# Kernel tuning notes

Measured on AMD Instinct MI355X. Metric: run time of the kernel, lower is better.

## Reference

```python
import jax, jax.numpy as jnp
import numpy as np

IN_DIM = 512
OUT_DIM = 128


def setup_inputs() -> dict:
    key = jax.random.key(0)
    ks = jax.random.split(key, 10)
    B, H, W = 8, 64, 64
    s_in = 1.0 / np.sqrt(IN_DIM)
    s_out = 1.0 / np.sqrt(OUT_DIM)
    return {
        "x": jax.random.normal(ks[0], (B, IN_DIM, H, W), dtype=jnp.float32),
        "W_in": jax.random.normal(ks[1], (OUT_DIM, IN_DIM), dtype=jnp.float32) * s_in,
        "b_in": jax.random.normal(ks[2], (OUT_DIM,), dtype=jnp.float32) * s_in,
        "W_q": jax.random.normal(ks[3], (OUT_DIM, OUT_DIM), dtype=jnp.float32) * s_out,
        "b_q": jax.random.normal(ks[4], (OUT_DIM,), dtype=jnp.float32) * s_out,
        "W_k": jax.random.normal(ks[5], (OUT_DIM, OUT_DIM), dtype=jnp.float32) * s_out,
        "b_k": jax.random.normal(ks[6], (OUT_DIM,), dtype=jnp.float32) * s_out,
        "W_v": jax.random.normal(ks[7], (OUT_DIM, OUT_DIM), dtype=jnp.float32) * s_out,
        "b_v": jax.random.normal(ks[8], (OUT_DIM,), dtype=jnp.float32) * s_out,
        "gamma": jax.random.normal(ks[9], (1,), dtype=jnp.float32) * 0.1,
    }


def reference(x, W_in, b_in, W_q, b_q, W_k, b_k, W_v, b_v, gamma):
    # 1x1 input projection: (B, C_in, H, W) -> (B, C, H, W)
    x = jnp.einsum('bihw,oi->bohw', x, W_in) + b_in[None, :, None, None]
    B, C, H, W = x.shape
    N = H * W
    xf = x.reshape(B, C, N)
    # 1x1 convs on flattened spatial dim are per-token matmuls
    q = jnp.einsum('bcn,oc->bon', xf, W_q) + b_q[None, :, None]  # (B, C, N)
    k = jnp.einsum('bcn,oc->bon', xf, W_k) + b_k[None, :, None]
    v = jnp.einsum('bcn,oc->bon', xf, W_v) + b_v[None, :, None]
    # energy[b, n, m] = sum_c q[b, c, n] * k[b, c, m]   (no 1/sqrt(d) scaling)
    energy = jnp.einsum('bcn,bcm->bnm', q, k)
    attention = jax.nn.softmax(energy, axis=-1)  # (B, N, N)
    # out[b, c, n] = sum_m v[b, c, m] * attention[b, n, m]  (V @ A^T)
    out = jnp.einsum('bcm,bnm->bcn', v, attention).reshape(B, C, H, W)
    return gamma * out + x
```

## Files before the change

kernel.cpp:

```cpp
#include <hip/hip_runtime.h>


typedef __attribute__((ext_vector_type(4))) float f32x4;
typedef __attribute__((ext_vector_type(8))) short bf16x8;
typedef __attribute__((ext_vector_type(4))) unsigned short u16x4;

#define MFMA16(a, b, c) __builtin_amdgcn_mfma_f32_16x16x32_bf16((a), (b), (c), 0, 0, 0)
#define LOG2E 1.44269504088896340736f
#define SOFTMAX_SHIFT 40.0f

#if __has_builtin(__builtin_amdgcn_exp2f)
#define EXP2F(x) __builtin_amdgcn_exp2f(x)
#else
#define EXP2F(x) exp2f(x)
#endif

__device__ __forceinline__ unsigned short f2bf(float f) {
  union { float f; unsigned int u; } v; v.f = f;
  unsigned int r = v.u + 0x7FFFu + ((v.u >> 16) & 1u);
  return (unsigned short)(r >> 16);
}

__device__ __forceinline__ void gload_lds16(const void* g, void* l) {
  __builtin_amdgcn_global_load_lds(
      (const __attribute__((address_space(1))) unsigned int*)(unsigned long long)g,
      (__attribute__((address_space(3))) unsigned int*)(unsigned int)(unsigned long long)l,
      16, 0, 0);
}

__global__ void cvt_w_kernel(const float* __restrict__ Win, const float* __restrict__ Wq,
                             const float* __restrict__ Wk, const float* __restrict__ Wv,
                             unsigned short* __restrict__ o) {
  int t = blockIdx.x * 256 + threadIdx.x;
  if (t < 65536)       o[t] = f2bf(Win[t]);
  else if (t < 81920)  o[t] = f2bf(Wq[t - 65536]);
  else if (t < 98304)  o[t] = f2bf(Wk[t - 81920]);
  else if (t < 114688) o[t] = f2bf(Wv[t - 98304]);
}

__global__ __launch_bounds__(256) void proj_in_kernel(
    const float* __restrict__ x, const unsigned short* __restrict__ Wb,
    const float* __restrict__ b_in, float* __restrict__ xf, unsigned short* __restrict__ xh) {
  __shared__ alignas(16) unsigned short xt[16 * 512];
  const int tid = threadIdx.x;
  const int w = tid >> 6, L = tid & 63, l15 = L & 15, qd = L >> 4;
  const int n0 = blockIdx.x * 64;
  const int b = blockIdx.y;
  const float* xb = x + (size_t)b * 512 * 4096;

  f32x4 acc[2][4];
#pragma unroll
  for (int ma = 0; ma < 2; ++ma)
#pragma unroll
    for (int nb = 0; nb < 4; ++nb) acc[ma][nb] = (f32x4){0.f, 0.f, 0.f, 0.f};

  for (int c4 = 0; c4 < 4; ++c4) {
    const int i0 = c4 * 128;
    __syncthreads();
    {
      const int nl = (tid & 15) * 4;
#pragma unroll
      for (int it = 0; it < 8; ++it) {
        const int il = (tid >> 4) + it * 16;
        f32x4 xv = *(const f32x4*)(xb + (size_t)(i0 + il) * 4096 + n0 + nl);
        const int kk = il >> 5, qr = (il >> 3) & 3, j = il & 7;
#pragma unroll
        for (int jj = 0; jj < 4; ++jj) {
          const int n_local = nl + jj;
          xt[(((n_local >> 4) << 2) + kk) * 512 + (qr * 16 + (n_local & 15)) * 8 + j] =
              f2bf(xv[jj]);
        }
      }
    }
    __syncthreads();
#pragma unroll
    for (int kk = 0; kk < 4; ++kk) {
      bf16x8 a[2];
#pragma unroll
      for (int ma = 0; ma < 2; ++ma)
        a[ma] = *(const bf16x8*)(Wb + (size_t)(w * 32 + ma * 16 + l15) * 512 + i0 + kk * 32 + qd * 8);
#pragma unroll
      for (int nb = 0; nb < 4; ++nb) {
        bf16x8 bf = *(const bf16x8*)&xt[(nb * 4 + kk) * 512 + L * 8];
#pragma unroll
        for (int ma = 0; ma < 2; ++ma) acc[ma][nb] = MFMA16(a[ma], bf, acc[ma][nb]);
      }
    }
  }
  float* xfb = xf + (size_t)b * 128 * 4096;
  unsigned short* xhb = xh + (size_t)b * 4096 * 128;
#pragma unroll
  for (int ma = 0; ma < 2; ++ma) {
    const int c0 = w * 32 + ma * 16 + qd * 4;
    const float bi0 = b_in[c0], bi1 = b_in[c0 + 1], bi2 = b_in[c0 + 2], bi3 = b_in[c0 + 3];
#pragma unroll
    for (int nb = 0; nb < 4; ++nb) {
      const int n = n0 + nb * 16 + l15;
      const float v0 = acc[ma][nb][0] + bi0, v1 = acc[ma][nb][1] + bi1;
      const float v2 = acc[ma][nb][2] + bi2, v3 = acc[ma][nb][3] + bi3;
      xfb[(size_t)(c0 + 0) * 4096 + n] = v0;
      xfb[(size_t)(c0 + 1) * 4096 + n] = v1;
      xfb[(size_t)(c0 + 2) * 4096 + n] = v2;
      xfb[(size_t)(c0 + 3) * 4096 + n] = v3;
      u16x4 h = {f2bf(v0), f2bf(v1), f2bf(v2), f2bf(v3)};
      *(u16x4*)&xhb[(size_t)n * 128 + c0] = h;
    }
  }
}

__global__ __launch_bounds__(256) void proj_qkv_kernel(
    const unsigned short* __restrict__ xh, const unsigned short* __restrict__ Wq,
    const float* __restrict__ bq, const unsigned short* __restrict__ Wk,
    const float* __restrict__ bk, const unsigned short* __restrict__ Wv,
    const float* __restrict__ bv, unsigned short* __restrict__ qt,
    unsigned short* __restrict__ kt, unsigned short* __restrict__ vv) {
  __shared__ alignas(16) unsigned short xt[32 * 512];
  const int tid = threadIdx.x;
  const int w = tid >> 6, L = tid & 63, l15 = L & 15, qd = L >> 4;
  const int n0 = blockIdx.x * 128;
  const int b = blockIdx.y;
  const unsigned short* xhb = xh + (size_t)b * 4096 * 128;

#pragma unroll
  for (int j = 0; j < 8; ++j) {
    const int blk = w * 8 + j;
    const int nb = blk >> 2, kk = blk & 3;
    const unsigned short* g = xhb + (size_t)(n0 + nb * 16 + l15) * 128 + kk * 32 + qd * 8;
    gload_lds16(g, &xt[blk * 512]);
  }
  __syncthreads();

  for (int which = 0; which < 2; ++which) {
    const unsigned short* W = which ? Wk : Wq;
    const float* bias = which ? bk : bq;
    unsigned short* dst = (which ? kt : qt) + (size_t)b * 4096 * 128;
    f32x4 acc[2][8];
#pragma unroll
    for (int ma = 0; ma < 2; ++ma)
#pragma unroll
      for (int nb = 0; nb < 8; ++nb) acc[ma][nb] = (f32x4){0.f, 0.f, 0.f, 0.f};
#pragma unroll
    for (int kk = 0; kk < 4; ++kk) {
      bf16x8 a[2];
#pragma unroll
      for (int ma = 0; ma < 2; ++ma)
        a[ma] = *(const bf16x8*)(W + (size_t)(w * 32 + ma * 16 + l15) * 128 + kk * 32 + qd * 8);
#pragma unroll
      for (int nb = 0; nb < 8; ++nb) {
        bf16x8 bf = *(const bf16x8*)&xt[(nb * 4 + kk) * 512 + L * 8];
#pragma unroll
        for (int ma = 0; ma < 2; ++ma) acc[ma][nb] = MFMA16(a[ma], bf, acc[ma][nb]);
      }
    }
#pragma unroll
    for (int ma = 0; ma < 2; ++ma) {
      const int c0 = w * 32 + ma * 16 + qd * 4;
      const float b0 = bias[c0], b1 = bias[c0 + 1], b2 = bias[c0 + 2], b3 = bias[c0 + 3];
#pragma unroll
      for (int nb = 0; nb < 8; ++nb) {
        const int n = n0 + nb * 16 + l15;
        u16x4 h = {f2bf(acc[ma][nb][0] + b0), f2bf(acc[ma][nb][1] + b1),
                   f2bf(acc[ma][nb][2] + b2), f2bf(acc[ma][nb][3] + b3)};
        *(u16x4*)&dst[(size_t)n * 128 + c0] = h;
      }
    }
  }
  {
    f32x4 acc[2][8];
#pragma unroll
    for (int ma = 0; ma < 2; ++ma)
#pragma unroll
      for (int cb = 0; cb < 8; ++cb) acc[ma][cb] = (f32x4){0.f, 0.f, 0.f, 0.f};
#pragma unroll
    for (int kk = 0; kk < 4; ++kk) {
      bf16x8 a[2];
#pragma unroll
      for (int ma = 0; ma < 2; ++ma)
        a[ma] = *(const bf16x8*)&xt[(((w * 2 + ma) << 2) + kk) * 512 + L * 8];
#pragma unroll
      for (int cb = 0; cb < 8; ++cb) {
        bf16x8 bf = *(const bf16x8*)(Wv + (size_t)(cb * 16 + l15) * 128 + kk * 32 + qd * 8);
#pragma unroll
        for (int ma = 0; ma < 2; ++ma) acc[ma][cb] = MFMA16(a[ma], bf, acc[ma][cb]);
      }
    }
    unsigned short* db = vv + (size_t)b * 128 * 4096;
#pragma unroll
    for (int ma = 0; ma < 2; ++ma) {
      const int nbase = n0 + w * 32 + ma * 16 + qd * 4;
#pragma unroll
      for (int cb = 0; cb < 8; ++cb) {
        const int c = cb * 16 + l15;
        const float bvv = bv[c];
        u16x4 h = {f2bf(acc[ma][cb][0] + bvv), f2bf(acc[ma][cb][1] + bvv),
                   f2bf(acc[ma][cb][2] + bvv), f2bf(acc[ma][cb][3] + bvv)};
        *(u16x4*)&db[(size_t)c * 4096 + nbase] = h;
      }
    }
  }
}

__global__ __launch_bounds__(256, 2) void attn_kernel(
    const unsigned short* __restrict__ qt, const unsigned short* __restrict__ kt,
    const unsigned short* __restrict__ vv, float* __restrict__ pa,
    float* __restrict__ lp, int nsplit) {
  __shared__ alignas(16) unsigned short kbuf[16 * 512];
  __shared__ alignas(16) unsigned short vbuf[16 * 512];
  __shared__ alignas(16) unsigned short pbuf[4][32][72];

  const int tid = threadIdx.x;
  const int w = tid >> 6, L = tid & 63, l15 = L & 15, qd = L >> 4;
  const int bidx = blockIdx.x;
  const int b = bidx & 7;
  const int r2 = bidx >> 3;
  const int qtile = r2 & 31, split = r2 >> 5;
  const int n00 = qtile * 128;
  const int mlen = 4096 / nsplit;
  const int mbeg = split * mlen;

  const unsigned short* qtb = qt + (size_t)b * 4096 * 128;
  const unsigned short* ktb = kt + (size_t)b * 4096 * 128;
  const unsigned short* vvb = vv + (size_t)b * 128 * 4096;

  bf16x8 qf[2][4];
#pragma unroll
  for (int nh = 0; nh < 2; ++nh) {
    const unsigned short* qrow = qtb + (size_t)(n00 + w * 32 + nh * 16 + l15) * 128 + qd * 8;
#pragma unroll
    for (int kk = 0; kk < 4; ++kk) qf[nh][kk] = *(const bf16x8*)(qrow + kk * 32);
  }

  f32x4 acc[2][8];
#pragma unroll
  for (int nh = 0; nh < 2; ++nh)
#pragma unroll
    for (int cb = 0; cb < 8; ++cb) acc[nh][cb] = (f32x4){0.f, 0.f, 0.f, 0.f};
  float lsum[2] = {0.f, 0.f};
  const float sb = SOFTMAX_SHIFT * LOG2E;

  for (int m0 = mbeg; m0 < mbeg + mlen; m0 += 64) {
    __syncthreads();
#pragma unroll
    for (int j = 0; j < 4; ++j) {
      const int blk = w * 4 + j;
      const int mb = blk >> 2, kk = blk & 3;
      gload_lds16(ktb + (size_t)(m0 + mb * 16 + l15) * 128 + kk * 32 + qd * 8,
                  &kbuf[blk * 512]);
      const int cb2 = blk >> 1, kkm = blk & 1;
      gload_lds16(vvb + (size_t)(cb2 * 16 + l15) * 4096 + m0 + kkm * 32 + qd * 8,
                  &vbuf[blk * 512]);
    }
    __syncthreads();

    f32x4 s[2][4];
#pragma unroll
    for (int mb = 0; mb < 4; ++mb) {
      s[0][mb] = (f32x4){0.f, 0.f, 0.f, 0.f};
      s[1][mb] = (f32x4){0.f, 0.f, 0.f, 0.f};
#pragma unroll
      for (int kk = 0; kk < 4; ++kk) {
        bf16x8 kf = *(const bf16x8*)&kbuf[(mb * 4 + kk) * 512 + L * 8];
        s[0][mb] = MFMA16(kf, qf[0][kk], s[0][mb]);
        s[1][mb] = MFMA16(kf, qf[1][kk], s[1][mb]);
      }
    }
#pragma unroll
    for (int nh = 0; nh < 2; ++nh) {
#pragma unroll
      for (int mb = 0; mb < 4; ++mb) {
        float p0 = EXP2F(__builtin_fmaf(s[nh][mb][0], LOG2E, -sb));
        float p1 = EXP2F(__builtin_fmaf(s[nh][mb][1], LOG2E, -sb));
        float p2 = EXP2F(__builtin_fmaf(s[nh][mb][2], LOG2E, -sb));
        float p3 = EXP2F(__builtin_fmaf(s[nh][mb][3], LOG2E, -sb));
        lsum[nh] += (p0 + p1) + (p2 + p3);
        u16x4 h = {f2bf(p0), f2bf(p1), f2bf(p2), f2bf(p3)};
        *(u16x4*)&pbuf[w][nh * 16 + l15][mb * 16 + qd * 4] = h;
      }
    }
#pragma unroll
    for (int kkm = 0; kkm < 2; ++kkm) {
      bf16x8 pf0 = *(const bf16x8*)&pbuf[w][l15][kkm * 32 + qd * 8];
      bf16x8 pf1 = *(const bf16x8*)&pbuf[w][16 + l15][kkm * 32 + qd * 8];
#pragma unroll
      for (int cb = 0; cb < 8; ++cb) {
        bf16x8 vf = *(const bf16x8*)&vbuf[(cb * 2 + kkm) * 512 + L * 8];
        acc[0][cb] = MFMA16(pf0, vf, acc[0][cb]);
        acc[1][cb] = MFMA16(pf1, vf, acc[1][cb]);
      }
    }
  }
#pragma unroll
  for (int nh = 0; nh < 2; ++nh) {
    lsum[nh] += __shfl_xor(lsum[nh], 16);
    lsum[nh] += __shfl_xor(lsum[nh], 32);
  }
  float* pab = pa + (size_t)(b * nsplit + split) * 4096 * 128;
#pragma unroll
  for (int nh = 0; nh < 2; ++nh) {
    const int nb_ = n00 + w * 32 + nh * 16 + qd * 4;
#pragma unroll
    for (int cb = 0; cb < 8; ++cb) {
      const int c = cb * 16 + l15;
#pragma unroll
      for (int r = 0; r < 4; ++r) pab[(size_t)(nb_ + r) * 128 + c] = acc[nh][cb][r];
    }
    if (L < 16) lp[(size_t)(b * nsplit + split) * 4096 + n00 + w * 32 + nh * 16 + l15] = lsum[nh];
  }
}

__global__ __launch_bounds__(256) void combine_kernel(
    const float* __restrict__ pa, const float* __restrict__ lp,
    const float* __restrict__ xf, const float* __restrict__ gamma_p,
    float* __restrict__ out, int nsplit) {
  __shared__ float tile[64 * 129];
  __shared__ float linv[64];
  const int tid = threadIdx.x;
  const int n0 = blockIdx.x * 64;
  const int b = blockIdx.y;

  const float* a0 = pa + ((size_t)(b * nsplit) * 4096 + n0) * 128;
#pragma unroll
  for (int i = 0; i < 8; ++i) {
    const int v = tid + i * 256;
    const int n = v >> 5, cw = (v & 31) * 4;
    f32x4 s = *(const f32x4*)(a0 + (size_t)n * 128 + cw);
    if (nsplit == 2) {
      f32x4 s2 = *(const f32x4*)(a0 + (size_t)4096 * 128 + (size_t)n * 128 + cw);
      s = s + s2;
    }
    float* t = &tile[n * 129 + cw];
    t[0] = s[0]; t[1] = s[1]; t[2] = s[2]; t[3] = s[3];
  }
  if (tid < 64) {
    float l = lp[(size_t)(b * nsplit) * 4096 + n0 + tid];
    if (nsplit == 2) l += lp[(size_t)(b * nsplit + 1) * 4096 + n0 + tid];
    linv[tid] = gamma_p[0] / l;
  }
  __syncthreads();
  const size_t ob = (size_t)b * 128 * 4096;
#pragma unroll
  for (int i = 0; i < 8; ++i) {
    const int v = tid + i * 256;
    const int c = v >> 4, nq = (v & 15) * 4;
    f32x4 xv = *(const f32x4*)(xf + ob + (size_t)c * 4096 + n0 + nq);
    f32x4 o;
#pragma unroll
    for (int j = 0; j < 4; ++j)
      o[j] = tile[(nq + j) * 129 + c] * linv[nq + j] + xv[j];
    *(f32x4*)(out + ob + (size_t)c * 4096 + n0 + nq) = o;
  }
}

extern "C" void kernel_launch(void* const* d_in, const int* in_sizes, int n_in,
                              void* d_out, int out_size, void* d_ws, size_t ws_size,
                              hipStream_t stream) {
  const float* x    = (const float*)d_in[0];
  const float* W_in = (const float*)d_in[1];
  const float* b_in = (const float*)d_in[2];
  const float* W_q  = (const float*)d_in[3];
  const float* b_q  = (const float*)d_in[4];
  const float* W_k  = (const float*)d_in[5];
  const float* b_k  = (const float*)d_in[6];
  const float* W_v  = (const float*)d_in[7];
  const float* b_v  = (const float*)d_in[8];
  const float* gam  = (const float*)d_in[9];
  float* out = (float*)d_out;

  char* ws = (char*)d_ws;
  unsigned short* Wb_in = (unsigned short*)ws;
  unsigned short* Wb_q  = Wb_in + 65536;
  unsigned short* Wb_k  = Wb_q + 16384;
  unsigned short* Wb_v  = Wb_k + 16384;
  float* xf          = (float*)(ws + 262144);
  unsigned short* xh = (unsigned short*)(ws + 262144 + 16777216);
  unsigned short* qt = xh + (size_t)8 * 4096 * 128;
  unsigned short* kt = qt + (size_t)8 * 4096 * 128;
  unsigned short* vv = kt + (size_t)8 * 4096 * 128;
  float* lp = (float*)(ws + 50593792);
  float* pa = lp + (size_t)8 * 2 * 4096;

  const size_t need2 = 50593792 + 262144 + (size_t)8 * 2 * 4096 * 128 * 4;
  const int nsplit = (ws_size >= need2) ? 2 : 1;

  cvt_w_kernel<<<448, 256, 0, stream>>>(W_in, W_q, W_k, W_v, Wb_in);
  proj_in_kernel<<<dim3(64, 8), 256, 0, stream>>>(x, Wb_in, b_in, xf, xh);
  proj_qkv_kernel<<<dim3(32, 8), 256, 0, stream>>>(xh, Wb_q, b_q, Wb_k, b_k, Wb_v, b_v,
                                                   qt, kt, vv);
  attn_kernel<<<256 * nsplit, 256, 0, stream>>>(qt, kt, vv, pa, lp, nsplit);
  combine_kernel<<<dim3(64, 8), 256, 0, stream>>>(pa, lp, xf, gam, out, nsplit);
}
```

Measured before the change: 262.9 us.

## Fuse input and QKV projections into one kernel and allow four-way KV split

Merges the input projection and the Q/K/V projections into a single 512-thread kernel. The bf16 copy of the projected activations now stays in LDS instead of round-tripping through global memory, removing one launch and the xh buffer traffic. LDS for the transposed input uses an XOR swizzle to cut bank conflicts, and bf16 packing switches to a cheaper perm-based conversion that rounds half away from zero instead of to even. The attention split can now go up to four ways when the workspace is large enough, raising parallelism at the cost of more partial-sum traffic in the combine step.

```diff
diff --git a/kernel.cpp b/kernel.cpp
--- a/kernel.cpp
+++ b/kernel.cpp
@@ -3,7 +3,8 @@
 
 typedef __attribute__((ext_vector_type(4))) float f32x4;
 typedef __attribute__((ext_vector_type(8))) short bf16x8;
-typedef __attribute__((ext_vector_type(4))) unsigned short u16x4;
+typedef __attribute__((ext_vector_type(2))) unsigned int u32x2;
+typedef __attribute__((ext_vector_type(4))) unsigned int u32x4;
 
 #define MFMA16(a, b, c) __builtin_amdgcn_mfma_f32_16x16x32_bf16((a), (b), (c), 0, 0, 0)
 #define LOG2E 1.44269504088896340736f
@@ -19,6 +20,12 @@
   union { float f; unsigned int u; } v; v.f = f;
   unsigned int r = v.u + 0x7FFFu + ((v.u >> 16) & 1u);
   return (unsigned short)(r >> 16);
+}
+
+__device__ __forceinline__ unsigned int pkbf(float a, float b) {
+  unsigned int ua = __float_as_uint(a) + 0x8000u;
+  unsigned int ub = __float_as_uint(b) + 0x8000u;
+  return __builtin_amdgcn_perm(ub, ua, 0x07060302u);
 }
 
 __device__ __forceinline__ void gload_lds16(const void* g, void* l) {
@@ -38,164 +45,124 @@
   else if (t < 114688) o[t] = f2bf(Wv[t - 98304]);
 }
 
-__global__ __launch_bounds__(256) void proj_in_kernel(
+__global__ __launch_bounds__(512) void proj_kernel(
     const float* __restrict__ x, const unsigned short* __restrict__ Wb,
-    const float* __restrict__ b_in, float* __restrict__ xf, unsigned short* __restrict__ xh) {
-  __shared__ alignas(16) unsigned short xt[16 * 512];
+    const float* __restrict__ b_in, const float* __restrict__ bq,
+    const float* __restrict__ bk, const float* __restrict__ bv,
+    float* __restrict__ xf, unsigned short* __restrict__ qt,
+    unsigned short* __restrict__ kt, unsigned short* __restrict__ vv) {
+  __shared__ alignas(16) unsigned short xt[32 * 512];
+  __shared__ alignas(16) unsigned short xt2[32 * 512];
   const int tid = threadIdx.x;
   const int w = tid >> 6, L = tid & 63, l15 = L & 15, qd = L >> 4;
-  const int n0 = blockIdx.x * 64;
+  const int n0 = blockIdx.x * 128;
   const int b = blockIdx.y;
   const float* xb = x + (size_t)b * 512 * 4096;
 
-  f32x4 acc[2][4];
-#pragma unroll
-  for (int ma = 0; ma < 2; ++ma)
-#pragma unroll
-    for (int nb = 0; nb < 4; ++nb) acc[ma][nb] = (f32x4){0.f, 0.f, 0.f, 0.f};
+  const int io = tid >> 5, nq = tid & 31;
+  const int il0 = io * 8, kkA = io >> 2, qr = io & 3;
+  const int nbA = nq >> 2;
+  const int Lsw8 = (L ^ ((L >> 2) & 7)) * 8;
+
+  f32x4 acc[8];
+#pragma unroll
+  for (int nb = 0; nb < 8; ++nb) acc[nb] = (f32x4){0.f, 0.f, 0.f, 0.f};
 
   for (int c4 = 0; c4 < 4; ++c4) {
     const int i0 = c4 * 128;
     __syncthreads();
-    {
-      const int nl = (tid & 15) * 4;
-#pragma unroll
-      for (int it = 0; it < 8; ++it) {
-        const int il = (tid >> 4) + it * 16;
-        f32x4 xv = *(const f32x4*)(xb + (size_t)(i0 + il) * 4096 + n0 + nl);
-        const int kk = il >> 5, qr = (il >> 3) & 3, j = il & 7;
-#pragma unroll
-        for (int jj = 0; jj < 4; ++jj) {
-          const int n_local = nl + jj;
-          xt[(((n_local >> 4) << 2) + kk) * 512 + (qr * 16 + (n_local & 15)) * 8 + j] =
-              f2bf(xv[jj]);
-        }
-      }
+    f32x4 xv[8];
+#pragma unroll
+    for (int r = 0; r < 8; ++r)
+      xv[r] = *(const f32x4*)(xb + (size_t)(i0 + il0 + r) * 4096 + n0 + nq * 4);
+#pragma unroll
+    for (int j = 0; j < 4; ++j) {
+      const int n15 = (nq & 3) * 4 + j;
+      const int s = qr * 16 + n15;
+      const int sp = s ^ ((s >> 2) & 7);
+      u32x4 d = {pkbf(xv[0][j], xv[1][j]), pkbf(xv[2][j], xv[3][j]),
+                 pkbf(xv[4][j], xv[5][j]), pkbf(xv[6][j], xv[7][j])};
+      *(u32x4*)&xt[(nbA * 4 + kkA) * 512 + sp * 8] = d;
     }
     __syncthreads();
 #pragma unroll
     for (int kk = 0; kk < 4; ++kk) {
-      bf16x8 a[2];
-#pragma unroll
-      for (int ma = 0; ma < 2; ++ma)
-        a[ma] = *(const bf16x8*)(Wb + (size_t)(w * 32 + ma * 16 + l15) * 512 + i0 + kk * 32 + qd * 8);
-#pragma unroll
-      for (int nb = 0; nb < 4; ++nb) {
-        bf16x8 bf = *(const bf16x8*)&xt[(nb * 4 + kk) * 512 + L * 8];
-#pragma unroll
-        for (int ma = 0; ma < 2; ++ma) acc[ma][nb] = MFMA16(a[ma], bf, acc[ma][nb]);
-      }
-    }
-  }
-  float* xfb = xf + (size_t)b * 128 * 4096;
-  unsigned short* xhb = xh + (size_t)b * 4096 * 128;
-#pragma unroll
-  for (int ma = 0; ma < 2; ++ma) {
-    const int c0 = w * 32 + ma * 16 + qd * 4;
+      bf16x8 a = *(const bf16x8*)(Wb + (size_t)(w * 16 + l15) * 512 + i0 + kk * 32 + qd * 8);
+#pragma unroll
+      for (int nb = 0; nb < 8; ++nb) {
+        bf16x8 bfv = *(const bf16x8*)&xt[(nb * 4 + kk) * 512 + Lsw8];
+        acc[nb] = MFMA16(a, bfv, acc[nb]);
+      }
+    }
+  }
+  {
+    const int c0 = w * 16 + qd * 4;
     const float bi0 = b_in[c0], bi1 = b_in[c0 + 1], bi2 = b_in[c0 + 2], bi3 = b_in[c0 + 3];
-#pragma unroll
-    for (int nb = 0; nb < 4; ++nb) {
+    float* xfb = xf + (size_t)b * 128 * 4096;
+    const int slot = ((w * 2 + (qd >> 1)) & 3) * 16 + l15;
+    const int blkb = (w >> 1);
+#pragma unroll
+    for (int nb = 0; nb < 8; ++nb) {
       const int n = n0 + nb * 16 + l15;
-      const float v0 = acc[ma][nb][0] + bi0, v1 = acc[ma][nb][1] + bi1;
-      const float v2 = acc[ma][nb][2] + bi2, v3 = acc[ma][nb][3] + bi3;
+      const float v0 = acc[nb][0] + bi0, v1 = acc[nb][1] + bi1;
+      const float v2 = acc[nb][2] + bi2, v3 = acc[nb][3] + bi3;
       xfb[(size_t)(c0 + 0) * 4096 + n] = v0;
       xfb[(size_t)(c0 + 1) * 4096 + n] = v1;
       xfb[(size_t)(c0 + 2) * 4096 + n] = v2;
       xfb[(size_t)(c0 + 3) * 4096 + n] = v3;
-      u16x4 h = {f2bf(v0), f2bf(v1), f2bf(v2), f2bf(v3)};
-      *(u16x4*)&xhb[(size_t)n * 128 + c0] = h;
-    }
-  }
-}
-
-__global__ __launch_bounds__(256) void proj_qkv_kernel(
-    const unsigned short* __restrict__ xh, const unsigned short* __restrict__ Wq,
-    const float* __restrict__ bq, const unsigned short* __restrict__ Wk,
-    const float* __restrict__ bk, const unsigned short* __restrict__ Wv,
-    const float* __restrict__ bv, unsigned short* __restrict__ qt,
-    unsigned short* __restrict__ kt, unsigned short* __restrict__ vv) {
-  __shared__ alignas(16) unsigned short xt[32 * 512];
-  const int tid = threadIdx.x;
-  const int w = tid >> 6, L = tid & 63, l15 = L & 15, qd = L >> 4;
-  const int n0 = blockIdx.x * 128;
-  const int b = blockIdx.y;
-  const unsigned short* xhb = xh + (size_t)b * 4096 * 128;
-
-#pragma unroll
-  for (int j = 0; j < 8; ++j) {
-    const int blk = w * 8 + j;
-    const int nb = blk >> 2, kk = blk & 3;
-    const unsigned short* g = xhb + (size_t)(n0 + nb * 16 + l15) * 128 + kk * 32 + qd * 8;
-    gload_lds16(g, &xt[blk * 512]);
+      u32x2 h = {pkbf(v0, v1), pkbf(v2, v3)};
+      *(u32x2*)&xt2[(nb * 4 + blkb) * 512 + slot * 8 + (qd & 1) * 4] = h;
+    }
   }
   __syncthreads();
 
   for (int which = 0; which < 2; ++which) {
-    const unsigned short* W = which ? Wk : Wq;
+    const unsigned short* W = Wb + 65536 + which * 16384;
     const float* bias = which ? bk : bq;
     unsigned short* dst = (which ? kt : qt) + (size_t)b * 4096 * 128;
-    f32x4 acc[2][8];
-#pragma unroll
-    for (int ma = 0; ma < 2; ++ma)
-#pragma unroll
-      for (int nb = 0; nb < 8; ++nb) acc[ma][nb] = (f32x4){0.f, 0.f, 0.f, 0.f};
+    f32x4 a2[8];
+#pragma unroll
+    for (int nb = 0; nb < 8; ++nb) a2[nb] = (f32x4){0.f, 0.f, 0.f, 0.f};
 #pragma unroll
     for (int kk = 0; kk < 4; ++kk) {
-      bf16x8 a[2];
-#pragma unroll
-      for (int ma = 0; ma < 2; ++ma)
-        a[ma] = *(const bf16x8*)(W + (size_t)(w * 32 + ma * 16 + l15) * 128 + kk * 32 + qd * 8);
+      bf16x8 a = *(const bf16x8*)(W + (size_t)(w * 16 + l15) * 128 + kk * 32 + qd * 8);
 #pragma unroll
       for (int nb = 0; nb < 8; ++nb) {
-        bf16x8 bf = *(const bf16x8*)&xt[(nb * 4 + kk) * 512 + L * 8];
-#pragma unroll
-        for (int ma = 0; ma < 2; ++ma) acc[ma][nb] = MFMA16(a[ma], bf, acc[ma][nb]);
-      }
-    }
-#pragma unroll
-    for (int ma = 0; ma < 2; ++ma) {
-      const int c0 = w * 32 + ma * 16 + qd * 4;
-      const float b0 = bias[c0], b1 = bias[c0 + 1], b2 = bias[c0 + 2], b3 = bias[c0 + 3];
-#pragma unroll
-      for (int nb = 0; nb < 8; ++nb) {
-        const int n = n0 + nb * 16 + l15;
-        u16x4 h = {f2bf(acc[ma][nb][0] + b0), f2bf(acc[ma][nb][1] + b1),
-                   f2bf(acc[ma][nb][2] + b2), f2bf(acc[ma][nb][3] + b3)};
-        *(u16x4*)&dst[(size_t)n * 128 + c0] = h;
-      }
+        bf16x8 bfv = *(const bf16x8*)&xt2[(nb * 4 + kk) * 512 + L * 8];
+        a2[nb] = MFMA16(a, bfv, a2[nb]);
+      }
+    }
+    const int c0 = w * 16 + qd * 4;
+    const float b0 = bias[c0], b1 = bias[c0 + 1], b2 = bias[c0 + 2], b3 = bias[c0 + 3];
+#pragma unroll
+    for (int nb = 0; nb < 8; ++nb) {
+      const int n = n0 + nb * 16 + l15;
+      u32x2 h = {pkbf(a2[nb][0] + b0, a2[nb][1] + b1), pkbf(a2[nb][2] + b2, a2[nb][3] + b3)};
+      *(u32x2*)&dst[(size_t)n * 128 + c0] = h;
     }
   }
   {
-    f32x4 acc[2][8];
-#pragma unroll
-    for (int ma = 0; ma < 2; ++ma)
-#pragma unroll
-      for (int cb = 0; cb < 8; ++cb) acc[ma][cb] = (f32x4){0.f, 0.f, 0.f, 0.f};
+    const unsigned short* Wv = Wb + 98304;
+    f32x4 a2[8];
+#pragma unroll
+    for (int cb = 0; cb < 8; ++cb) a2[cb] = (f32x4){0.f, 0.f, 0.f, 0.f};
 #pragma unroll
     for (int kk = 0; kk < 4; ++kk) {
-      bf16x8 a[2];
-#pragma unroll
-      for (int ma = 0; ma < 2; ++ma)
-        a[ma] = *(const bf16x8*)&xt[(((w * 2 + ma) << 2) + kk) * 512 + L * 8];
+      bf16x8 a = *(const bf16x8*)&xt2[(w * 4 + kk) * 512 + L * 8];
 #pragma unroll
       for (int cb = 0; cb < 8; ++cb) {
-        bf16x8 bf = *(const bf16x8*)(Wv + (size_t)(cb * 16 + l15) * 128 + kk * 32 + qd * 8);
-#pragma unroll
-        for (int ma = 0; ma < 2; ++ma) acc[ma][cb] = MFMA16(a[ma], bf, acc[ma][cb]);
+        bf16x8 bfv = *(const bf16x8*)(Wv + (size_t)(cb * 16 + l15) * 128 + kk * 32 + qd * 8);
+        a2[cb] = MFMA16(a, bfv, a2[cb]);
       }
     }
     unsigned short* db = vv + (size_t)b * 128 * 4096;
-#pragma unroll
-    for (int ma = 0; ma < 2; ++ma) {
-      const int nbase = n0 + w * 32 + ma * 16 + qd * 4;
-#pragma unroll
-      for (int cb = 0; cb < 8; ++cb) {
-        const int c = cb * 16 + l15;
-        const float bvv = bv[c];
-        u16x4 h = {f2bf(acc[ma][cb][0] + bvv), f2bf(acc[ma][cb][1] + bvv),
-                   f2bf(acc[ma][cb][2] + bvv), f2bf(acc[ma][cb][3] + bvv)};
-        *(u16x4*)&db[(size_t)c * 4096 + nbase] = h;
-      }
+    const int nbase = n0 + w * 16 + qd * 4;
+#pragma unroll
+    for (int cb = 0; cb < 8; ++cb) {
+      const int c = cb * 16 + l15;
+      const float bvv = bv[c];
+      u32x2 h = {pkbf(a2[cb][0] + bvv, a2[cb][1] + bvv), pkbf(a2[cb][2] + bvv, a2[cb][3] + bvv)};
+      *(u32x2*)&db[(size_t)c * 4096 + nbase] = h;
     }
   }
 }
@@ -273,8 +240,8 @@
         float p2 = EXP2F(__builtin_fmaf(s[nh][mb][2], LOG2E, -sb));
         float p3 = EXP2F(__builtin_fmaf(s[nh][mb][3], LOG2E, -sb));
         lsum[nh] += (p0 + p1) + (p2 + p3);
-        u16x4 h = {f2bf(p0), f2bf(p1), f2bf(p2), f2bf(p3)};
-        *(u16x4*)&pbuf[w][nh * 16 + l15][mb * 16 + qd * 4] = h;
+        u32x2 h = {pkbf(p0, p1), pkbf(p2, p3)};
+        *(u32x2*)&pbuf[w][nh * 16 + l15][mb * 16 + qd * 4] = h;
       }
     }
 #pragma unroll
@@ -324,16 +291,15 @@
     const int v = tid + i * 256;
     const int n = v >> 5, cw = (v & 31) * 4;
     f32x4 s = *(const f32x4*)(a0 + (size_t)n * 128 + cw);
-    if (nsplit == 2) {
-      f32x4 s2 = *(const f32x4*)(a0 + (size_t)4096 * 128 + (size_t)n * 128 + cw);
-      s = s + s2;
-    }
+    for (int sp = 1; sp < nsplit; ++sp)
+      s += *(const f32x4*)(a0 + (size_t)sp * 4096 * 128 + (size_t)n * 128 + cw);
     float* t = &tile[n * 129 + cw];
     t[0] = s[0]; t[1] = s[1]; t[2] = s[2]; t[3] = s[3];
   }
   if (tid < 64) {
-    float l = lp[(size_t)(b * nsplit) * 4096 + n0 + tid];
-    if (nsplit == 2) l += lp[(size_t)(b * nsplit + 1) * 4096 + n0 + tid];
+    float l = 0.f;
+    for (int sp = 0; sp < nsplit; ++sp)
+      l += lp[(size_t)(b * nsplit + sp) * 4096 + n0 + tid];
     linv[tid] = gamma_p[0] / l;
   }
   __syncthreads();
@@ -367,25 +333,22 @@
   float* out = (float*)d_out;
 
   char* ws = (char*)d_ws;
-  unsigned short* Wb_in = (unsigned short*)ws;
-  unsigned short* Wb_q  = Wb_in + 65536;
-  unsigned short* Wb_k  = Wb_q + 16384;
-  unsigned short* Wb_v  = Wb_k + 16384;
+  unsigned short* Wb = (unsigned short*)ws;
   float* xf          = (float*)(ws + 262144);
-  unsigned short* xh = (unsigned short*)(ws + 262144 + 16777216);
-  unsigned short* qt = xh + (size_t)8 * 4096 * 128;
+  unsigned short* qt = (unsigned short*)(ws + 262144 + 16777216);
   unsigned short* kt = qt + (size_t)8 * 4096 * 128;
   unsigned short* vv = kt + (size_t)8 * 4096 * 128;
-  float* lp = (float*)(ws + 50593792);
-  float* pa = lp + (size_t)8 * 2 * 4096;
-
-  const size_t need2 = 50593792 + 262144 + (size_t)8 * 2 * 4096 * 128 * 4;
-  const int nsplit = (ws_size >= need2) ? 2 : 1;
-
-  cvt_w_kernel<<<448, 256, 0, stream>>>(W_in, W_q, W_k, W_v, Wb_in);
-  proj_in_kernel<<<dim3(64, 8), 256, 0, stream>>>(x, Wb_in, b_in, xf, xh);
-  proj_qkv_kernel<<<dim3(32, 8), 256, 0, stream>>>(xh, Wb_q, b_q, Wb_k, b_k, Wb_v, b_v,
-                                                   qt, kt, vv);
+  const size_t base_end = 262144 + 16777216 + 3ull * 8388608;
+  float* lp = (float*)(ws + base_end);
+  float* pa = lp + (size_t)8 * 4 * 4096;
+
+  const size_t fixed = base_end + 524288;
+  const int nsplit = (ws_size >= fixed + 4ull * 16777216) ? 4
+                   : (ws_size >= fixed + 2ull * 16777216) ? 2 : 1;
+
+  cvt_w_kernel<<<448, 256, 0, stream>>>(W_in, W_q, W_k, W_v, Wb);
+  proj_kernel<<<dim3(32, 8), 512, 0, stream>>>(x, Wb, b_in, b_q, b_k, b_v,
+                                               xf, qt, kt, vv);
   attn_kernel<<<256 * nsplit, 256, 0, stream>>>(qt, kt, vv, pa, lp, nsplit);
   combine_kernel<<<dim3(64, 8), 256, 0, stream>>>(pa, lp, xf, gam, out, nsplit);
 }
```

Result: faster. 251.0 us (-4.5%).
